# Performance work log

Hardware: AMD Instinct MI355X
Metric: run time of the kernel (lower is better)

The kernel has to match this reference:

```python
import jax, jax.numpy as jnp
import numpy as np

H, F, D, E, L = 8, 768, 128, 256, 13   # heads, feat_dim, compression_dim, embed_dim, nb_layer
B, T = 8, 1000
DCOR = D * (D - 1) // 2                # 8128, upper-triangle (offset=1) correlation features


def setup_inputs() -> dict:
    key = jax.random.key(0)
    ks = jax.random.split(key, 12)
    s = lambda k, shape, sc=0.02: jax.random.normal(k, shape, jnp.float32) * sc
    return {
        "x": jax.random.normal(ks[0], (B, F, T, L), jnp.float32),
        "weights_k": jnp.ones((H, L), jnp.float32),
        "weights_v": jnp.ones((H, L), jnp.float32),
        "q": jax.random.normal(ks[1], (H, D), jnp.float32),
        "Wk": s(ks[2], (H, D, F)), "bk": s(ks[3], (H, D)),
        "Wv": s(ks[4], (H, D, F)), "bv": s(ks[5], (H, D)),
        "Wproj": s(ks[6], (H, E, DCOR)), "bproj": s(ks[7], (H, E)),
        "WT": s(ks[8], (E, H * D)), "bT": s(ks[9], (E,)),
        "Wp": s(ks[10], (E, H * E)), "bp": s(ks[11], (E,)),
    }


def _norm_t(z):
    # normalize over the time axis; torch .var() is unbiased (ddof=1)
    mu = z.mean(axis=2, keepdims=True)
    sd = jnp.sqrt(z.var(axis=2, keepdims=True, ddof=1)) + 1e-9
    return (z - mu) / sd


def _forward(x, weights_k, weights_v, q, Wk, bk, Wv, bv, Wproj, bproj, WT, bT, Wp, bp):
    # x: [B, F, T, L]; per-head softmax-weighted layer sum -> [B, H, T, F]
    kw = jax.nn.softmax(weights_k, axis=-1)  # [H, L]
    vw = jax.nn.softmax(weights_v, axis=-1)
    k_raw = jnp.einsum('bftl,hl->bhtf', x, kw)
    v_raw = jnp.einsum('bftl,hl->bhtf', x, vw)
    # per-head compression linears -> [B, H, T, D]
    mh_k = jnp.einsum('bhtf,hdf->bhtd', k_raw, Wk) + bk[None, :, None, :]
    mh_v = jnp.einsum('bhtf,hdf->bhtd', v_raw, Wv) + bv[None, :, None, :]
    # single-query scaled-dot-product attention pooling per head
    scores = jnp.einsum('hd,bhtd->bht', q, mh_k) / jnp.sqrt(jnp.float32(D))
    attn = jax.nn.softmax(scores, axis=-1)
    o1 = jnp.einsum('bht,bhtd->bhd', attn, mh_v)           # [B, H, D]
    out_T = o1.reshape(B, H * D) @ WT.T + bT               # [B, E]
    # correlation branch (mh_q = mh_v): time-normalize, D x D correlation, triu(offset=1)
    k_n = _norm_t(mh_k)
    q_n = _norm_t(mh_v)
    corr = jnp.einsum('bhtk,bhtl->bhkl', k_n, q_n) / T     # [B, H, D, D]
    iu0, iu1 = np.triu_indices(D, k=1)
    mh_corr = corr[:, :, iu0, iu1]                         # [B, H, DCOR]
    outs = jnp.einsum('bhc,hec->bhe', mh_corr, Wproj) + bproj[None]
    out_F = outs.reshape(B, H * E) @ Wp.T + bp             # [B, E]
    return 0.5 * out_F + 0.5 * out_T


def reference(x, weights_k, weights_v, q, Wk, bk, Wv, bv, Wproj, bproj, WT, bT, Wp, bp):
    return _forward(x, weights_k, weights_v, q, Wk, bk, Wv, bv, Wproj, bproj, WT, bT, Wp, bp)
```

## Files before the change

### kernel.cpp

```cpp
#include <hip/hip_runtime.h>
#include <hip/hip_bf16.h>

#define Hn 8
#define Fn 768
#define Dn 128
#define En 256
#define Ln 13
#define Bn 8
#define Tn 1000
#define TPn 1024
#define NCOR 8128

typedef float f32x4 __attribute__((ext_vector_type(4)));
typedef __bf16 bf16x8 __attribute__((ext_vector_type(8)));
typedef unsigned short u16;

static __device__ __forceinline__ u16 f2bf(float f) {
  __hip_bfloat16 h = __float2bfloat16(f);
  return __builtin_bit_cast(u16, h);
}
static __device__ __forceinline__ float bf2f(u16 u) {
  return __bfloat162float(__builtin_bit_cast(__hip_bfloat16, u));
}

static __device__ __forceinline__ void gload_lds16(const u16* g, u16* lds_wave_base) {
  __builtin_amdgcn_global_load_lds(
      (const __attribute__((address_space(1))) unsigned int*)g,
      (__attribute__((address_space(3))) unsigned int*)lds_wave_base, 16, 0, 0);
}

__global__ __launch_bounds__(256) void k1_raw(
    const float* __restrict__ x,
    const float* __restrict__ wk, const float* __restrict__ wv,
    const float* __restrict__ Wk, const float* __restrict__ Wv,
    u16* __restrict__ kv_raw, u16* __restrict__ Wbf,
    float* __restrict__ s1, float* __restrict__ s2,
    int b0, int BG) {
  __shared__ float kvw[16 * Ln];
  __shared__ u16 res[16 * 32 * 34];
  int tid = threadIdx.x;
  if (tid < 16) {
    int kvi = tid >> 3, h = tid & 7;
    const float* w = (kvi ? wv : wk) + h * Ln;
    float m = -1e30f;
    for (int l = 0; l < Ln; ++l) m = fmaxf(m, w[l]);
    float e[Ln], s = 0.f;
    for (int l = 0; l < Ln; ++l) { e[l] = expf(w[l] - m); s += e[l]; }
    for (int l = 0; l < Ln; ++l) kvw[tid * Ln + l] = e[l] / s;
  }
  if (b0 == 0) {
    int nb = gridDim.x * gridDim.y * gridDim.z;
    int lin = blockIdx.x + gridDim.x * (blockIdx.y + gridDim.y * blockIdx.z);
    int n = 2 * Hn * Dn * Fn;
    for (int i = lin * 256 + tid; i < n; i += nb * 256) {
      float v = (i < Hn * Dn * Fn) ? Wk[i] : Wv[i - Hn * Dn * Fn];
      Wbf[i] = f2bf(v);
    }
    int ns = 2 * Bn * Hn * Dn;
    for (int i = lin * 256 + tid; i < ns; i += nb * 256) { s1[i] = 0.f; s2[i] = 0.f; }
  }
  int f0 = blockIdx.x * 32, t0 = blockIdx.y * 32;
  int b_l = blockIdx.z, b = b0 + b_l;
  int fl = tid & 31, tq = tid >> 5;
  int tbase = t0 + tq * 4;
  bool valid = (tbase < Tn);
  float4 xq[13];
  if (valid) {
    const float4* xp = (const float4*)(x + ((size_t)(b * Fn + f0 + fl) * Tn + tbase) * Ln);
#pragma unroll
    for (int i = 0; i < 13; ++i) xq[i] = xp[i];
  }
  __syncthreads();
  const float* xf = (const float*)xq;
  for (int o = 0; o < 16; ++o) {
    float a0 = 0.f, a1 = 0.f, a2 = 0.f, a3 = 0.f;
    if (valid) {
#pragma unroll
      for (int l = 0; l < Ln; ++l) {
        float w = kvw[o * Ln + l];
        a0 += xf[l] * w;
        a1 += xf[Ln + l] * w;
        a2 += xf[2 * Ln + l] * w;
        a3 += xf[3 * Ln + l] * w;
      }
    }
    int rb = o * 1088 + tq * 4 * 34 + fl;
    res[rb] = f2bf(a0);
    res[rb + 34] = f2bf(a1);
    res[rb + 68] = f2bf(a2);
    res[rb + 102] = f2bf(a3);
  }
  __syncthreads();
  int part = tid & 3;
#pragma unroll
  for (int it = 0; it < 8; ++it) {
    int r = (tid >> 2) + it * 64;
    int o = r >> 5, tl = r & 31;
    int kv = o >> 3, h = o & 7;
    const u16* src = res + o * 1088 + tl * 34 + part * 8;
    uint4 v;
    v.x = *(const unsigned*)(src + 0);
    v.y = *(const unsigned*)(src + 2);
    v.z = *(const unsigned*)(src + 4);
    v.w = *(const unsigned*)(src + 6);
    u16* dst = kv_raw + (((size_t)(kv * BG + b_l) * Hn + h) * TPn + t0 + tl) * Fn + f0 + part * 8;
    *reinterpret_cast<uint4*>(dst) = v;
  }
}

__global__ __launch_bounds__(256) void k2_gemm(
    const u16* __restrict__ kv_raw, const u16* __restrict__ Wbf,
    const float* __restrict__ bk, const float* __restrict__ bv,
    const float* __restrict__ qg,
    u16* __restrict__ mhT, float* __restrict__ s1buf, float* __restrict__ s2buf,
    float* __restrict__ scores, int b0, int BG) {
  __shared__ __align__(16) char ldsbuf[33280];
  __shared__ float qsh[Dn];
  u16* As0 = (u16*)ldsbuf;
  u16* Bs0 = (u16*)(ldsbuf + 8192);
  u16* As1 = (u16*)(ldsbuf + 16384);
  u16* Bs1 = (u16*)(ldsbuf + 24576);
  u16* Cst = (u16*)ldsbuf;
  int tid = threadIdx.x, lane = tid & 63, w = tid >> 6;
  int t0 = blockIdx.x * 128;
  int b_l = blockIdx.y / Hn, h = blockIdx.y % Hn, kv = blockIdx.z;
  int b = b0 + b_l;
  if (tid < Dn) qsh[tid] = qg[h * Dn + tid];
  const u16* Abase = kv_raw + ((size_t)(kv * BG + b_l) * Hn + h) * TPn * Fn + (size_t)t0 * Fn;
  const u16* Bbase = Wbf + ((size_t)(kv * Hn + h)) * Dn * Fn;
  f32x4 acc[4][4];
#pragma unroll
  for (int mi = 0; mi < 4; ++mi)
#pragma unroll
    for (int ni = 0; ni < 4; ++ni) acc[mi][ni] = (f32x4){0.f, 0.f, 0.f, 0.f};
  int wm = (w >> 1) * 64, wn = (w & 1) * 64;
  int lin0 = tid, lin1 = tid + 256;
  int row0 = lin0 >> 2, part0 = lin0 & 3;
  int row1 = lin1 >> 2, part1 = lin1 & 3;
  int wb0 = (w * 64) * 8, wb1 = (256 + w * 64) * 8;

  auto STAGE = [&](int f0, u16* Ad, u16* Bd) {
    gload_lds16(Abase + (size_t)row0 * Fn + f0 + part0 * 8, Ad + wb0);
    gload_lds16(Abase + (size_t)row1 * Fn + f0 + part1 * 8, Ad + wb1);
    gload_lds16(Bbase + (size_t)row0 * Fn + f0 + part0 * 8, Bd + wb0);
    gload_lds16(Bbase + (size_t)row1 * Fn + f0 + part1 * 8, Bd + wb1);
  };
  auto COMPUTE = [&](const u16* Ac, const u16* Bc) {
    bf16x8 af[4], bg[4];
#pragma unroll
    for (int mi = 0; mi < 4; ++mi)
      af[mi] = *(const bf16x8*)(Ac + (wm + mi * 16 + (lane & 15)) * 32 + (lane >> 4) * 8);
#pragma unroll
    for (int ni = 0; ni < 4; ++ni)
      bg[ni] = *(const bf16x8*)(Bc + (wn + ni * 16 + (lane & 15)) * 32 + (lane >> 4) * 8);
#pragma unroll
    for (int mi = 0; mi < 4; ++mi)
#pragma unroll
      for (int ni = 0; ni < 4; ++ni)
        acc[mi][ni] = __builtin_amdgcn_mfma_f32_16x16x32_bf16(af[mi], bg[ni], acc[mi][ni], 0, 0, 0);
  };

  STAGE(0, As0, Bs0);
  __syncthreads();
  for (int f0 = 0; f0 < Fn; f0 += 64) {
    if (f0 + 32 < Fn) STAGE(f0 + 32, As1, Bs1);
    COMPUTE(As0, Bs0);
    __syncthreads();
    if (f0 + 64 < Fn) STAGE(f0 + 64, As0, Bs0);
    COMPUTE(As1, Bs1);
    __syncthreads();
  }

  float bias[4];
  const float* bptr = (kv ? bv : bk) + h * Dn;
#pragma unroll
  for (int ni = 0; ni < 4; ++ni) bias[ni] = bptr[wn + ni * 16 + (lane & 15)];
#pragma unroll
  for (int mi = 0; mi < 4; ++mi)
#pragma unroll
    for (int ni = 0; ni < 4; ++ni)
#pragma unroll
      for (int r = 0; r < 4; ++r) {
        int row = wm + mi * 16 + (lane >> 4) * 4 + r;
        int col = wn + ni * 16 + (lane & 15);
        float v = acc[mi][ni][r] + bias[ni];
        if (t0 + row >= Tn) v = 0.f;
        Cst[row * 130 + col] = f2bf(v);
      }
  __syncthreads();
  int d = tid >> 1, half = tid & 1;
  u16* orow = mhT + (((size_t)(kv * Bn + b) * Hn + h) * Dn + d) * TPn + t0;
  float ssum = 0.f, ssq = 0.f;
#pragma unroll
  for (int j = 0; j < 8; ++j) {
    int tb = half * 64 + j * 8;
    u16 pk[8];
#pragma unroll
    for (int ii = 0; ii < 8; ++ii) {
      u16 ub = Cst[(tb + ii) * 130 + d];
      pk[ii] = ub;
      float vr = bf2f(ub);
      ssum += vr;
      ssq += vr * vr;
    }
    uint4 v4;
    v4.x = (unsigned)pk[0] | ((unsigned)pk[1] << 16);
    v4.y = (unsigned)pk[2] | ((unsigned)pk[3] << 16);
    v4.z = (unsigned)pk[4] | ((unsigned)pk[5] << 16);
    v4.w = (unsigned)pk[6] | ((unsigned)pk[7] << 16);
    *reinterpret_cast<uint4*>(orow + tb) = v4;
  }
  int sidx = ((kv * Bn + b) * Hn + h) * Dn + d;
  atomicAdd(&s1buf[sidx], ssum);
  atomicAdd(&s2buf[sidx], ssq);

  if (kv == 0) {
    int t = tid >> 1, hf = tid & 1;
    float s = 0.f;
    const u16* crow = Cst + t * 130 + hf * 64;
    const float* qh = qsh + hf * 64;
#pragma unroll
    for (int dd = 0; dd < 64; ++dd) s += qh[dd] * bf2f(crow[dd]);
    s += __shfl_xor(s, 1);
    if (hf == 0)
      scores[((size_t)b * Hn + h) * TPn + t0 + t] =
          (t0 + t < Tn) ? s * 0.088388347648318447f : -1e30f;
  }
}

__global__ __launch_bounds__(256) void k34(
    const u16* __restrict__ mhT, const float* __restrict__ scores,
    float* __restrict__ o1, float* __restrict__ Sgp) {
  __shared__ float sc[TPn];
  __shared__ float red[256];
  __shared__ __align__(16) u16 As0[4096], Bs0[4096], As1[4096], Bs1[4096];
  int tid = threadIdx.x;
  if (blockIdx.x < 256) {
    int bh = blockIdx.x >> 2, dq = blockIdx.x & 3;
    int b = bh >> 3, h = bh & 7;
    const float* srow = scores + (size_t)bh * TPn;
    float4 z4 = *((const float4*)srow + tid);
    float z[4] = {z4.x, z4.y, z4.z, z4.w};
    float m = fmaxf(fmaxf(z[0], z[1]), fmaxf(z[2], z[3]));
    red[tid] = m;
    __syncthreads();
    for (int s = 128; s > 0; s >>= 1) { if (tid < s) red[tid] = fmaxf(red[tid], red[tid + s]); __syncthreads(); }
    m = red[0];
    __syncthreads();
    float lsum = 0.f;
#pragma unroll
    for (int j = 0; j < 4; ++j) {
      float e = __expf(z[j] - m);
      sc[tid * 4 + j] = e;
      lsum += e;
    }
    red[tid] = lsum;
    __syncthreads();
    for (int s = 128; s > 0; s >>= 1) { if (tid < s) red[tid] += red[tid + s]; __syncthreads(); }
    float inv = 1.f / red[0];
    int dl = tid & 31, slice = tid >> 5;
    int d = dq * 32 + dl;
    const u16* Vr = mhT + ((size_t)(1 * Bn + b) * Hn + h) * Dn * TPn + (size_t)d * TPn + slice * 128;
    const float* at = sc + slice * 128;
    float a = 0.f;
#pragma unroll
    for (int i = 0; i < 16; ++i) {
      bf16x8 vv = *(const bf16x8*)(Vr + i * 8);
#pragma unroll
      for (int j = 0; j < 8; ++j) a += at[i * 8 + j] * (float)vv[j];
    }
    __syncthreads();
    red[tid] = a;
    __syncthreads();
    for (int s = 128; s >= 32; s >>= 1) { if (tid < s) red[tid] += red[tid + s]; __syncthreads(); }
    if (tid < 32) o1[((size_t)b * Hn + h) * Dn + dq * 32 + tid] = inv * red[tid];
    return;
  }
  int id = blockIdx.x - 256;
  int lane = tid & 63, w = tid >> 6;
  int bh = id & 63, tc = id >> 6;
  int b = bh >> 3, h = bh & 7;
  const u16* Kb = mhT + ((size_t)(0 * Bn + b) * Hn + h) * Dn * TPn;
  const u16* Vb = mhT + ((size_t)(1 * Bn + b) * Hn + h) * Dn * TPn;
  f32x4 acc[4][4];
#pragma unroll
  for (int mi = 0; mi < 4; ++mi)
#pragma unroll
    for (int ni = 0; ni < 4; ++ni) acc[mi][ni] = (f32x4){0.f, 0.f, 0.f, 0.f};
  int wm = (w >> 1) * 64, wn = (w & 1) * 64;
  int lin0 = tid, lin1 = tid + 256;
  int row0 = lin0 >> 2, part0 = lin0 & 3;
  int row1 = lin1 >> 2, part1 = lin1 & 3;
  int wb0 = (w * 64) * 8, wb1 = (256 + w * 64) * 8;
  int tb = tc * 256;

  auto STAGE = [&](int t0, u16* Ad, u16* Bd) {
    gload_lds16(Kb + (size_t)row0 * TPn + t0 + part0 * 8, Ad + wb0);
    gload_lds16(Kb + (size_t)row1 * TPn + t0 + part1 * 8, Ad + wb1);
    gload_lds16(Vb + (size_t)row0 * TPn + t0 + part0 * 8, Bd + wb0);
    gload_lds16(Vb + (size_t)row1 * TPn + t0 + part1 * 8, Bd + wb1);
  };
  auto COMPUTE = [&](const u16* Ac, const u16* Bc) {
    bf16x8 af[4], bg[4];
#pragma unroll
    for (int mi = 0; mi < 4; ++mi)
      af[mi] = *(const bf16x8*)(Ac + (wm + mi * 16 + (lane & 15)) * 32 + (lane >> 4) * 8);
#pragma unroll
    for (int ni = 0; ni < 4; ++ni)
      bg[ni] = *(const bf16x8*)(Bc + (wn + ni * 16 + (lane & 15)) * 32 + (lane >> 4) * 8);
#pragma unroll
    for (int mi = 0; mi < 4; ++mi)
#pragma unroll
      for (int ni = 0; ni < 4; ++ni)
        acc[mi][ni] = __builtin_amdgcn_mfma_f32_16x16x32_bf16(af[mi], bg[ni], acc[mi][ni], 0, 0, 0);
  };

  STAGE(tb, As0, Bs0);
  __syncthreads();
  for (int s = 0; s < 256; s += 64) {
    if (s + 32 < 256) STAGE(tb + s + 32, As1, Bs1);
    COMPUTE(As0, Bs0);
    __syncthreads();
    if (s + 64 < 256) STAGE(tb + s + 64, As0, Bs0);
    COMPUTE(As1, Bs1);
    __syncthreads();
  }
  float* dst = Sgp + ((size_t)tc * 64 + bh) * 16384;
#pragma unroll
  for (int mi = 0; mi < 4; ++mi)
#pragma unroll
    for (int ni = 0; ni < 4; ++ni)
#pragma unroll
      for (int r = 0; r < 4; ++r) {
        int mm = wm + mi * 16 + (lane >> 4) * 4 + r;
        int nn = wn + ni * 16 + (lane & 15);
        dst[mm * 128 + nn] = acc[mi][ni][r];
      }
}

__global__ __launch_bounds__(256) void k4b_corr(
    const float* __restrict__ Sgp, const float* __restrict__ s1buf,
    const float* __restrict__ s2buf, float* __restrict__ corr) {
  __shared__ float mkS[32], skS[32], mvS[128], svS[128];
  int tid = threadIdx.x;
  int bh = blockIdx.x >> 2, quad = blockIdx.x & 3;
  int b = bh >> 3, h = bh & 7;
  if (tid < 32) {
    int dd = quad * 32 + tid;
    int sidx = ((0 * Bn + b) * Hn + h) * Dn + dd;
    float a1 = s1buf[sidx], a2 = s2buf[sidx];
    float mu = a1 / (float)Tn;
    float var = (a2 - a1 * a1 / (float)Tn) / (float)(Tn - 1);
    mkS[tid] = mu;
    skS[tid] = sqrtf(fmaxf(var, 0.f)) + 1e-9f;
  } else if (tid < 160) {
    int dd = tid - 32;
    int sidx = ((1 * Bn + b) * Hn + h) * Dn + dd;
    float a1 = s1buf[sidx], a2 = s2buf[sidx];
    float mu = a1 / (float)Tn;
    float var = (a2 - a1 * a1 / (float)Tn) / (float)(Tn - 1);
    mvS[dd] = mu;
    svS[dd] = sqrtf(fmaxf(var, 0.f)) + 1e-9f;
  }
  __syncthreads();
  const float invT = 1.f / (float)Tn;
#pragma unroll
  for (int it = 0; it < 16; ++it) {
    int cell = it * 256 + tid;
    int ml = cell >> 7, nn = cell & 127;
    int mm = quad * 32 + ml;
    if (nn > mm) {
      size_t off = (size_t)bh * 16384 + mm * 128 + nn;
      float S = Sgp[off] + Sgp[off + (size_t)64 * 16384] +
                Sgp[off + (size_t)128 * 16384] + Sgp[off + (size_t)192 * 16384];
      float cv = (S - (float)Tn * mkS[ml] * mvS[nn]) * invT / (skS[ml] * svS[nn]);
      int cidx = mm * (2 * Dn - mm - 1) / 2 + (nn - mm - 1);
      corr[(size_t)bh * NCOR + cidx] = cv;
    }
  }
}

__global__ __launch_bounds__(256) void k5_proj(
    const float* __restrict__ corr, const float* __restrict__ Wproj,
    const float* __restrict__ bproj, float* __restrict__ outs) {
  __shared__ float red[8 * 256];
  int tid = threadIdx.x;
  int e = blockIdx.x, h = blockIdx.y;
  const float4* wp4 = (const float4*)(Wproj + ((size_t)h * En + e) * NCOR);
  float accs[8];
#pragma unroll
  for (int b = 0; b < 8; ++b) accs[b] = 0.f;
  for (int k = 0; k < 8; ++k) {
    int c4 = tid + k * 256;
    if (c4 < NCOR / 4) {
      float4 wv = wp4[c4];
#pragma unroll
      for (int b = 0; b < 8; ++b) {
        float4 cv = *((const float4*)(corr + ((size_t)b * Hn + h) * NCOR) + c4);
        accs[b] += wv.x * cv.x + wv.y * cv.y + wv.z * cv.z + wv.w * cv.w;
      }
    }
  }
#pragma unroll
  for (int b = 0; b < 8; ++b) red[b * 256 + tid] = accs[b];
  __syncthreads();
  for (int s = 128; s > 0; s >>= 1) {
    if (tid < s) {
#pragma unroll
      for (int b = 0; b < 8; ++b) red[b * 256 + tid] += red[b * 256 + tid + s];
    }
    __syncthreads();
  }
  if (tid < 8) outs[((size_t)tid * Hn + h) * En + e] = red[tid * 256] + bproj[h * En + e];
}

__global__ __launch_bounds__(256) void k5_final(
    const float* __restrict__ outs, const float* __restrict__ o1,
    const float* __restrict__ WT, const float* __restrict__ bT,
    const float* __restrict__ Wp, const float* __restrict__ bp,
    float* __restrict__ out) {
  __shared__ float os[2048];
  __shared__ float o1s[1024];
  __shared__ float redF[256], redT[256];
  int tid = threadIdx.x;
  int b = blockIdx.x >> 3, ic = blockIdx.x & 7;
  for (int i = tid; i < 2048; i += 256) os[i] = outs[(size_t)b * 2048 + i];
  for (int i = tid; i < 1024; i += 256) o1s[i] = o1[(size_t)b * 1024 + i];
  __syncthreads();
  int il = tid >> 3, slice = tid & 7;
  int i = ic * 32 + il;
  const float* wpr = Wp + (size_t)i * 2048;
  const float* wtr = WT + (size_t)i * 1024;
  float aF = 0.f, aT = 0.f;
  for (int kk = 0; kk < 256; ++kk) { int j = kk * 8 + slice; aF += os[j] * wpr[j]; }
  for (int kk = 0; kk < 128; ++kk) { int j = kk * 8 + slice; aT += o1s[j] * wtr[j]; }
  redF[tid] = aF; redT[tid] = aT;
  __syncthreads();
  for (int s = 4; s > 0; s >>= 1) {
    if (slice < s) { redF[tid] += redF[tid + s]; redT[tid] += redT[tid + s]; }
    __syncthreads();
  }
  if (slice == 0) {
    float oF = redF[tid] + bp[i];
    float oT = redT[tid] + bT[i];
    out[(size_t)b * En + i] = 0.5f * oF + 0.5f * oT;
  }
}

extern "C" void kernel_launch(void* const* d_in, const int* in_sizes, int n_in,
                              void* d_out, int out_size, void* d_ws, size_t ws_size,
                              hipStream_t stream) {
  const float* x     = (const float*)d_in[0];
  const float* wk    = (const float*)d_in[1];
  const float* wv    = (const float*)d_in[2];
  const float* q     = (const float*)d_in[3];
  const float* Wk    = (const float*)d_in[4];
  const float* bk    = (const float*)d_in[5];
  const float* Wv    = (const float*)d_in[6];
  const float* bv    = (const float*)d_in[7];
  const float* Wproj = (const float*)d_in[8];
  const float* bproj = (const float*)d_in[9];
  const float* WT    = (const float*)d_in[10];
  const float* bT    = (const float*)d_in[11];
  const float* Wp    = (const float*)d_in[12];
  const float* bp    = (const float*)d_in[13];
  float* out = (float*)d_out;

  char* ws = (char*)d_ws;
  size_t off = 0;
  auto alloc = [&](size_t bytes) { size_t p = off; off += (bytes + 255) & ~(size_t)255; return p; };
  u16*   Wbf    = (u16*)  (ws + alloc((size_t)2 * Hn * Dn * Fn * 2));
  u16*   mhT    = (u16*)  (ws + alloc((size_t)2 * Bn * Hn * Dn * TPn * 2));
  float* s1     = (float*)(ws + alloc((size_t)2 * Bn * Hn * Dn * 4));
  float* s2     = (float*)(ws + alloc((size_t)2 * Bn * Hn * Dn * 4));
  float* o1     = (float*)(ws + alloc((size_t)Bn * Hn * Dn * 4));
  float* corr   = (float*)(ws + alloc((size_t)Bn * Hn * NCOR * 4));
  float* outs   = (float*)(ws + alloc((size_t)Bn * Hn * En * 4));
  float* scores = (float*)(ws + alloc((size_t)Bn * Hn * TPn * 4));
  float* Sgp    = (float*)(ws + alloc((size_t)4 * Bn * Hn * Dn * Dn * 4));
  size_t fixed = off;
  size_t per_b = (size_t)2 * Hn * TPn * Fn * 2;
  int BG = 8;
  while (BG > 1 && fixed + (size_t)BG * per_b > ws_size) BG >>= 1;
  u16* kv_raw = (u16*)(ws + fixed);

  for (int b0 = 0; b0 < Bn; b0 += BG) {
    k1_raw<<<dim3(24, 32, BG), 256, 0, stream>>>(x, wk, wv, Wk, Wv, kv_raw, Wbf, s1, s2, b0, BG);
    k2_gemm<<<dim3(8, Hn * BG, 2), 256, 0, stream>>>(kv_raw, Wbf, bk, bv, q, mhT, s1, s2,
                                                     scores, b0, BG);
  }
  k34<<<512, 256, 0, stream>>>(mhT, scores, o1, Sgp);
  k4b_corr<<<256, 256, 0, stream>>>(Sgp, s1, s2, corr);
  k5_proj<<<dim3(En, Hn), 256, 0, stream>>>(corr, Wproj, bproj, outs);
  k5_final<<<64, 256, 0, stream>>>(outs, o1, WT, bT, Wp, bp, out);
}
```

Measured before the change: 669.8 us.

## Fuse correlation normalization into k34 by splitting over row quarters instead of time chunks

The correlation GEMM blocks change from splitting the time axis into four partial 128x128 sums to each computing a 32-row slice over the full time range. The time-normalization and triangle extraction epilogue is then applied directly from registers, which removes the Sgp partial-sum buffer and the separate k4b_corr launch. In exchange, each block runs a longer serial K loop with smaller MFMA tiles (2x2 per wave) and reloads the full V matrix four times across blocks. The mean/std shared-memory setup now relies on the loop's first barrier for synchronization.

```diff
diff --git a/kernel.cpp b/kernel.cpp
--- a/kernel.cpp
+++ b/kernel.cpp
@@ -230,10 +230,12 @@
 
 __global__ __launch_bounds__(256) void k34(
     const u16* __restrict__ mhT, const float* __restrict__ scores,
-    float* __restrict__ o1, float* __restrict__ Sgp) {
+    const float* __restrict__ s1buf, const float* __restrict__ s2buf,
+    float* __restrict__ o1, float* __restrict__ corr) {
   __shared__ float sc[TPn];
   __shared__ float red[256];
-  __shared__ __align__(16) u16 As0[4096], Bs0[4096], As1[4096], Bs1[4096];
+  __shared__ __align__(16) u16 Kt0[1024], Vt0[4096], Kt1[1024], Vt1[4096];
+  __shared__ float mkS[32], skS[32], mvS[128], svS[128];
   int tid = threadIdx.x;
   if (blockIdx.x < 256) {
     int bh = blockIdx.x >> 2, dq = blockIdx.x & 3;
@@ -278,75 +280,12 @@
   }
   int id = blockIdx.x - 256;
   int lane = tid & 63, w = tid >> 6;
-  int bh = id & 63, tc = id >> 6;
+  int bh = id & 63, rq = id >> 6;
   int b = bh >> 3, h = bh & 7;
-  const u16* Kb = mhT + ((size_t)(0 * Bn + b) * Hn + h) * Dn * TPn;
+  const u16* Kb = mhT + ((size_t)(0 * Bn + b) * Hn + h) * Dn * TPn + (size_t)(rq * 32) * TPn;
   const u16* Vb = mhT + ((size_t)(1 * Bn + b) * Hn + h) * Dn * TPn;
-  f32x4 acc[4][4];
-#pragma unroll
-  for (int mi = 0; mi < 4; ++mi)
-#pragma unroll
-    for (int ni = 0; ni < 4; ++ni) acc[mi][ni] = (f32x4){0.f, 0.f, 0.f, 0.f};
-  int wm = (w >> 1) * 64, wn = (w & 1) * 64;
-  int lin0 = tid, lin1 = tid + 256;
-  int row0 = lin0 >> 2, part0 = lin0 & 3;
-  int row1 = lin1 >> 2, part1 = lin1 & 3;
-  int wb0 = (w * 64) * 8, wb1 = (256 + w * 64) * 8;
-  int tb = tc * 256;
-
-  auto STAGE = [&](int t0, u16* Ad, u16* Bd) {
-    gload_lds16(Kb + (size_t)row0 * TPn + t0 + part0 * 8, Ad + wb0);
-    gload_lds16(Kb + (size_t)row1 * TPn + t0 + part1 * 8, Ad + wb1);
-    gload_lds16(Vb + (size_t)row0 * TPn + t0 + part0 * 8, Bd + wb0);
-    gload_lds16(Vb + (size_t)row1 * TPn + t0 + part1 * 8, Bd + wb1);
-  };
-  auto COMPUTE = [&](const u16* Ac, const u16* Bc) {
-    bf16x8 af[4], bg[4];
-#pragma unroll
-    for (int mi = 0; mi < 4; ++mi)
-      af[mi] = *(const bf16x8*)(Ac + (wm + mi * 16 + (lane & 15)) * 32 + (lane >> 4) * 8);
-#pragma unroll
-    for (int ni = 0; ni < 4; ++ni)
-      bg[ni] = *(const bf16x8*)(Bc + (wn + ni * 16 + (lane & 15)) * 32 + (lane >> 4) * 8);
-#pragma unroll
-    for (int mi = 0; mi < 4; ++mi)
-#pragma unroll
-      for (int ni = 0; ni < 4; ++ni)
-        acc[mi][ni] = __builtin_amdgcn_mfma_f32_16x16x32_bf16(af[mi], bg[ni], acc[mi][ni], 0, 0, 0);
-  };
-
-  STAGE(tb, As0, Bs0);
-  __syncthreads();
-  for (int s = 0; s < 256; s += 64) {
-    if (s + 32 < 256) STAGE(tb + s + 32, As1, Bs1);
-    COMPUTE(As0, Bs0);
-    __syncthreads();
-    if (s + 64 < 256) STAGE(tb + s + 64, As0, Bs0);
-    COMPUTE(As1, Bs1);
-    __syncthreads();
-  }
-  float* dst = Sgp + ((size_t)tc * 64 + bh) * 16384;
-#pragma unroll
-  for (int mi = 0; mi < 4; ++mi)
-#pragma unroll
-    for (int ni = 0; ni < 4; ++ni)
-#pragma unroll
-      for (int r = 0; r < 4; ++r) {
-        int mm = wm + mi * 16 + (lane >> 4) * 4 + r;
-        int nn = wn + ni * 16 + (lane & 15);
-        dst[mm * 128 + nn] = acc[mi][ni][r];
-      }
-}
-
-__global__ __launch_bounds__(256) void k4b_corr(
-    const float* __restrict__ Sgp, const float* __restrict__ s1buf,
-    const float* __restrict__ s2buf, float* __restrict__ corr) {
-  __shared__ float mkS[32], skS[32], mvS[128], svS[128];
-  int tid = threadIdx.x;
-  int bh = blockIdx.x >> 2, quad = blockIdx.x & 3;
-  int b = bh >> 3, h = bh & 7;
   if (tid < 32) {
-    int dd = quad * 32 + tid;
+    int dd = rq * 32 + tid;
     int sidx = ((0 * Bn + b) * Hn + h) * Dn + dd;
     float a1 = s1buf[sidx], a2 = s2buf[sidx];
     float mu = a1 / (float)Tn;
@@ -362,22 +301,65 @@
     mvS[dd] = mu;
     svS[dd] = sqrtf(fmaxf(var, 0.f)) + 1e-9f;
   }
-  __syncthreads();
+  f32x4 acc[2][2];
+#pragma unroll
+  for (int mi = 0; mi < 2; ++mi)
+#pragma unroll
+    for (int ni = 0; ni < 2; ++ni) acc[mi][ni] = (f32x4){0.f, 0.f, 0.f, 0.f};
+  int rowK = tid >> 2, partK = tid & 3;
+  int wbK = (w * 64) * 8;
+  int rowV0 = tid >> 2, partV0 = tid & 3;
+  int rowV1 = (tid + 256) >> 2, partV1 = tid & 3;
+  int wbV0 = (w * 64) * 8, wbV1 = (256 + w * 64) * 8;
+
+  auto STAGE = [&](int t0, u16* Kd, u16* Vd) {
+    if (w < 2)
+      gload_lds16(Kb + (size_t)rowK * TPn + t0 + partK * 8, Kd + wbK);
+    gload_lds16(Vb + (size_t)rowV0 * TPn + t0 + partV0 * 8, Vd + wbV0);
+    gload_lds16(Vb + (size_t)rowV1 * TPn + t0 + partV1 * 8, Vd + wbV1);
+  };
+  auto COMPUTE = [&](const u16* Kc, const u16* Vc) {
+    bf16x8 af[2], bg[2];
+#pragma unroll
+    for (int mi = 0; mi < 2; ++mi)
+      af[mi] = *(const bf16x8*)(Kc + (mi * 16 + (lane & 15)) * 32 + (lane >> 4) * 8);
+#pragma unroll
+    for (int ni = 0; ni < 2; ++ni)
+      bg[ni] = *(const bf16x8*)(Vc + (w * 32 + ni * 16 + (lane & 15)) * 32 + (lane >> 4) * 8);
+#pragma unroll
+    for (int mi = 0; mi < 2; ++mi)
+#pragma unroll
+      for (int ni = 0; ni < 2; ++ni)
+        acc[mi][ni] = __builtin_amdgcn_mfma_f32_16x16x32_bf16(af[mi], bg[ni], acc[mi][ni], 0, 0, 0);
+  };
+
+  STAGE(0, Kt0, Vt0);
+  __syncthreads();
+  for (int s = 0; s < TPn; s += 64) {
+    if (s + 32 < TPn) STAGE(s + 32, Kt1, Vt1);
+    COMPUTE(Kt0, Vt0);
+    __syncthreads();
+    if (s + 64 < TPn) STAGE(s + 64, Kt0, Vt0);
+    COMPUTE(Kt1, Vt1);
+    __syncthreads();
+  }
   const float invT = 1.f / (float)Tn;
 #pragma unroll
-  for (int it = 0; it < 16; ++it) {
-    int cell = it * 256 + tid;
-    int ml = cell >> 7, nn = cell & 127;
-    int mm = quad * 32 + ml;
-    if (nn > mm) {
-      size_t off = (size_t)bh * 16384 + mm * 128 + nn;
-      float S = Sgp[off] + Sgp[off + (size_t)64 * 16384] +
-                Sgp[off + (size_t)128 * 16384] + Sgp[off + (size_t)192 * 16384];
-      float cv = (S - (float)Tn * mkS[ml] * mvS[nn]) * invT / (skS[ml] * svS[nn]);
-      int cidx = mm * (2 * Dn - mm - 1) / 2 + (nn - mm - 1);
-      corr[(size_t)bh * NCOR + cidx] = cv;
-    }
-  }
+  for (int mi = 0; mi < 2; ++mi)
+#pragma unroll
+    for (int ni = 0; ni < 2; ++ni)
+#pragma unroll
+      for (int r = 0; r < 4; ++r) {
+        int ml = mi * 16 + (lane >> 4) * 4 + r;
+        int nn = w * 32 + ni * 16 + (lane & 15);
+        int mm = rq * 32 + ml;
+        if (nn > mm) {
+          float S = acc[mi][ni][r];
+          float cv = (S - (float)Tn * mkS[ml] * mvS[nn]) * invT / (skS[ml] * svS[nn]);
+          int cidx = mm * (2 * Dn - mm - 1) / 2 + (nn - mm - 1);
+          corr[(size_t)bh * NCOR + cidx] = cv;
+        }
+      }
 }
 
 __global__ __launch_bounds__(256) void k5_proj(
@@ -477,7 +459,6 @@
   float* corr   = (float*)(ws + alloc((size_t)Bn * Hn * NCOR * 4));
   float* outs   = (float*)(ws + alloc((size_t)Bn * Hn * En * 4));
   float* scores = (float*)(ws + alloc((size_t)Bn * Hn * TPn * 4));
-  float* Sgp    = (float*)(ws + alloc((size_t)4 * Bn * Hn * Dn * Dn * 4));
   size_t fixed = off;
   size_t per_b = (size_t)2 * Hn * TPn * Fn * 2;
   int BG = 8;
@@ -489,8 +470,7 @@
     k2_gemm<<<dim3(8, Hn * BG, 2), 256, 0, stream>>>(kv_raw, Wbf, bk, bv, q, mhT, s1, s2,
                                                      scores, b0, BG);
   }
-  k34<<<512, 256, 0, stream>>>(mhT, scores, o1, Sgp);
-  k4b_corr<<<256, 256, 0, stream>>>(Sgp, s1, s2, corr);
+  k34<<<512, 256, 0, stream>>>(mhT, scores, s1, s2, o1, corr);
   k5_proj<<<dim3(En, Hn), 256, 0, stream>>>(corr, Wproj, bproj, outs);
   k5_final<<<64, 256, 0, stream>>>(outs, o1, WT, bT, Wp, bp, out);
 }
```

Result: no change. 668.0 us (-0.3%).
